# Kernel optimization log

Measured on AMD Instinct MI355X. Metric: run time of the kernel, lower is better.

The kernel has to match this reference:

```python
import jax, jax.numpy as jnp
import numpy as np

B, C, H, W = 32, 1024, 28, 28
TEXT_DIM = 768
ATTN_DIM = 256
REDUCTION = 16
RED = max(1, C // REDUCTION)


def setup_inputs() -> dict:
    key = jax.random.key(0)
    ks = jax.random.split(key, 8)
    x = jax.random.normal(ks[0], (B, C, H, W), dtype=jnp.float32)
    text_feat = jax.random.normal(ks[1], (B, TEXT_DIM), dtype=jnp.float32)
    # ChannelAttention shared MLP (Linear weights, torch layout [out, in], no bias)
    w1 = jax.random.normal(ks[2], (RED, C), dtype=jnp.float32) * (1.0 / np.sqrt(C))
    w2 = jax.random.normal(ks[3], (C, RED), dtype=jnp.float32) * (1.0 / np.sqrt(RED))
    # TextGuidedSpatialAttention projections
    wq = jax.random.normal(ks[4], (ATTN_DIM, TEXT_DIM), dtype=jnp.float32) * 0.001
    wk = jax.random.normal(ks[5], (ATTN_DIM, C), dtype=jnp.float32) * np.sqrt(2.0 / ATTN_DIM)
    wv = jax.random.normal(ks[6], (ATTN_DIM, C), dtype=jnp.float32) * np.sqrt(2.0 / ATTN_DIM)
    wo = jax.random.normal(ks[7], (1, ATTN_DIM), dtype=jnp.float32) * np.sqrt(2.0)
    return {"x": x, "text_feat": text_feat, "w1": w1, "w2": w2,
            "wq": wq, "wk": wk, "wv": wv, "wo": wo}


def _forward(x, text_feat, w1, w2, wq, wk, wv, wo):
    b, c, h, w = x.shape
    # ----- Channel attention -----
    avg = jnp.mean(x, axis=(2, 3))          # [B, C]
    mx = jnp.max(x, axis=(2, 3))            # [B, C]
    def mlp(z):
        return jax.nn.relu(z @ w1.T) @ w2.T  # [B, C]
    ch_attn = jax.nn.sigmoid(mlp(avg) + mlp(mx))   # [B, C]
    x = x * ch_attn[:, :, None, None]
    # ----- Text-guided spatial attention -----
    q = text_feat @ wq.T                     # [B, A]
    # 1x1 conv == channel contraction
    k = jnp.einsum('ac,bchw->bahw', wk, x).reshape(b, ATTN_DIM, h * w)  # [B, A, N]
    v = jnp.einsum('ac,bchw->bahw', wv, x).reshape(b, ATTN_DIM, h * w)  # [B, A, N]
    scores = jnp.einsum('ba,ban->bn', q, k) / jnp.sqrt(jnp.float32(ATTN_DIM))  # [B, N]
    attn_weights = jax.nn.softmax(scores, axis=-1)                      # [B, N]
    attended = jnp.einsum('bn,ban->ba', attn_weights, v)                # [B, A]
    # out_proj 1x1 conv on a spatially-constant tensor == scalar per batch, broadcast
    spatial_scalar = jax.nn.sigmoid(attended @ wo.T)                    # [B, 1]
    spatial_attn = jnp.broadcast_to(spatial_scalar[:, :, None, None], (b, 1, h, w))
    return x * spatial_attn, spatial_attn


def reference(x, text_feat, w1, w2, wq, wk, wv, wo):
    return _forward(x, text_feat, w1, w2, wq, wk, wv, wo)
```

## Files before the change

### kernel.cpp

```cpp
#include <hip/hip_runtime.h>
#include <math.h>

#define B_   32
#define C_   1024
#define N_   784
#define NF4  196
#define TD   768
#define AD   256
#define RED_ 64
#define OUT0 25690112
#define ROWS (B_*C_)
#define CH_  16
#define CPB  64

typedef float f4 __attribute__((ext_vector_type(4)));

#define OFF_AVG 0
#define OFF_MAX 32768
#define OFF_CA  65536
#define OFF_Q   98304
#define OFF_HS  106496
#define OFF_WVO 108544
#define OFF_GQ  109568
#define OFF_SV  142336
#define OFF_CNT 142368
#define OFF_S   142400
#define OFF_Y   167488

__global__ void k_avgmax(const float* __restrict__ x, const float* __restrict__ text,
                         const float* __restrict__ wq, float* __restrict__ avg,
                         float* __restrict__ mx, float* __restrict__ q,
                         int* __restrict__ cnt, float* __restrict__ S,
                         float* __restrict__ Y) {
    int blk = blockIdx.x;
    int wave = threadIdx.x >> 6, lane = threadIdx.x & 63;
    if (blk < 4096) {
        int row0 = blk * 8 + wave * 2;
        const float4* r0 = (const float4*)(x + (size_t)row0 * N_);
        const float4* r1 = r0 + NF4;
        float s0 = 0.f, s1 = 0.f, m0 = -3.4e38f, m1 = -3.4e38f;
        #pragma unroll
        for (int j = 0; j < 3; ++j) {
            int i = lane + 64 * j;
            float4 v0 = r0[i], v1 = r1[i];
            s0 += v0.x + v0.y + v0.z + v0.w;
            s1 += v1.x + v1.y + v1.z + v1.w;
            m0 = fmaxf(m0, fmaxf(fmaxf(v0.x, v0.y), fmaxf(v0.z, v0.w)));
            m1 = fmaxf(m1, fmaxf(fmaxf(v1.x, v1.y), fmaxf(v1.z, v1.w)));
        }
        if (lane < 4) {
            float4 v0 = r0[192 + lane], v1 = r1[192 + lane];
            s0 += v0.x + v0.y + v0.z + v0.w;
            s1 += v1.x + v1.y + v1.z + v1.w;
            m0 = fmaxf(m0, fmaxf(fmaxf(v0.x, v0.y), fmaxf(v0.z, v0.w)));
            m1 = fmaxf(m1, fmaxf(fmaxf(v1.x, v1.y), fmaxf(v1.z, v1.w)));
        }
        for (int o = 32; o; o >>= 1) {
            s0 += __shfl_down(s0, o, 64);
            s1 += __shfl_down(s1, o, 64);
            m0 = fmaxf(m0, __shfl_down(m0, o, 64));
            m1 = fmaxf(m1, __shfl_down(m1, o, 64));
        }
        if (lane == 0) {
            avg[row0]     = s0 * (1.f / (float)N_); mx[row0]     = m0;
            avg[row0 + 1] = s1 * (1.f / (float)N_); mx[row0 + 1] = m1;
        }
    } else if (blk < 6144) {
        int w = (blk - 4096) * 4 + wave;
        int b = w >> 8, a = w & 255;
        const float4* tb = (const float4*)(text + (size_t)b * TD);
        const float4* wr = (const float4*)(wq + (size_t)a * TD);
        float acc = 0.f;
        #pragma unroll
        for (int j = 0; j < 3; ++j) {
            int i = lane + 64 * j;
            float4 tv = tb[i], wvv = wr[i];
            acc += tv.x * wvv.x + tv.y * wvv.y + tv.z * wvv.z + tv.w * wvv.w;
        }
        for (int o = 32; o; o >>= 1) acc += __shfl_down(acc, o, 64);
        if (lane == 0) q[(size_t)b * AD + a] = acc;
    } else if (blk < 6169) {
        int idx = (blk - 6144) * 256 + threadIdx.x;
        if (idx < 6272) {
            f4 z = {0.f, 0.f, 0.f, 0.f};
            ((f4*)S)[idx] = z; ((f4*)Y)[idx] = z;
        }
    } else {
        if (threadIdx.x < B_) cnt[threadIdx.x] = 0;
    }
}

__global__ void k_proj(const float* __restrict__ avg, const float* __restrict__ mx,
                       const float* __restrict__ w1, const float* __restrict__ q,
                       const float* __restrict__ wk, const float* __restrict__ wv,
                       const float* __restrict__ wo, float* __restrict__ hs,
                       float* __restrict__ gq, float* __restrict__ wvo) {
    int blk  = blockIdx.x;
    int wave = threadIdx.x >> 6, lane = threadIdx.x & 63;
    int t = threadIdx.x;
    __shared__ float red[256];
    __shared__ float qs[AD];
    if (blk < 512) {
        int w = blk * 4 + wave;
        int b = w >> 6, r = w & 63;
        const float4* av = (const float4*)(avg + (size_t)b * C_);
        const float4* mv = (const float4*)(mx + (size_t)b * C_);
        const float4* wr = (const float4*)(w1 + (size_t)r * C_);
        float aa = 0.f, am = 0.f;
        #pragma unroll
        for (int j = 0; j < 4; ++j) {
            int i = lane + 64 * j;
            float4 wvv = wr[i], a4 = av[i], m4 = mv[i];
            aa += wvv.x * a4.x + wvv.y * a4.y + wvv.z * a4.z + wvv.w * a4.w;
            am += wvv.x * m4.x + wvv.y * m4.y + wvv.z * m4.z + wvv.w * m4.w;
        }
        for (int o = 32; o; o >>= 1) {
            aa += __shfl_down(aa, o, 64);
            am += __shfl_down(am, o, 64);
        }
        if (lane == 0) hs[(size_t)b * RED_ + r] = fmaxf(aa, 0.f) + fmaxf(am, 0.f);
    } else if (blk < 1024) {
        int local = blk - 512;
        int b  = local >> 4, cb = local & 15;
        int cl = t & 63, sl = t >> 6;
        int c  = cb * 64 + cl;
        qs[t] = q[(size_t)b * AD + t];
        __syncthreads();
        const float* wkp = wk + (size_t)(sl * 64) * C_ + c;
        float acc = 0.f;
        #pragma unroll 8
        for (int a = 0; a < 64; ++a) acc += qs[sl * 64 + a] * wkp[(size_t)a * C_];
        red[t] = acc;
        __syncthreads();
        if (t < 64) gq[(size_t)b * C_ + c] = red[t] + red[64 + t] + red[128 + t] + red[192 + t];
    } else {
        int local = blk - 1024;
        int cl = t & 63, sl = t >> 6;
        int c = local * 64 + cl;
        const float* wvp = wv + (size_t)(sl * 64) * C_ + c;
        float acc = 0.f;
        #pragma unroll 8
        for (int a = 0; a < 64; ++a) acc += wo[sl * 64 + a] * wvp[(size_t)a * C_];
        red[t] = acc;
        __syncthreads();
        if (t < 64) wvo[local * 64 + t] = red[t] + red[64 + t] + red[128 + t] + red[192 + t];
    }
}

__global__ __launch_bounds__(256, 4) void k_scores(
        const float* __restrict__ x, const float* __restrict__ hs,
        const float* __restrict__ w2, const float* __restrict__ gq,
        const float* __restrict__ wvo,
        float* __restrict__ ca, float* __restrict__ S, float* __restrict__ Y,
        int* __restrict__ cnt, float* __restrict__ sv) {
    int chunk = blockIdx.x;
    int bh    = blockIdx.y;
    int b = bh >> 1, half = bh & 1;
    int t = threadIdx.x;
    int wave = t >> 6, lane = t & 63;
    __shared__ float hss[RED_];
    __shared__ float redB[256];
    __shared__ float gsg[CPB], gsh[CPB];
    __shared__ f4 l4s[392], l4y[392];
    __shared__ float rm[4], rs[4], rd[4];
    __shared__ int winflag;

    if (t < RED_) hss[t] = hs[(size_t)b * RED_ + t];
    __syncthreads();
    {
        int cl = t & 63, sl = t >> 6;
        int c  = chunk * CPB + cl;
        const float* w2p = w2 + (size_t)c * RED_ + sl * 16;
        float a1 = 0.f;
        #pragma unroll
        for (int r = 0; r < 16; ++r) a1 += hss[sl * 16 + r] * w2p[r];
        redB[t] = a1;
    }
    __syncthreads();
    if (t < CPB) {
        float s1 = redB[t] + redB[64 + t] + redB[128 + t] + redB[192 + t];
        float cav = 1.f / (1.f + __expf(-s1));
        int c = chunk * CPB + t;
        ca[(size_t)b * C_ + c] = cav;
        gsg[t] = gq[(size_t)b * C_ + c] * cav * 0.0625f;
        gsh[t] = wvo[c] * cav;
    }
    __syncthreads();
    const f4* xb4 = (const f4*)(x +
        ((size_t)b * C_ + (size_t)chunk * CPB + (size_t)wave * 16) * N_) + (size_t)half * 98;
    f4 sA = {0,0,0,0}, sB = {0,0,0,0}, yA = {0,0,0,0}, yB = {0,0,0,0};
    #pragma unroll 4
    for (int cc = 0; cc < 16; ++cc) {
        float gv = gsg[wave * 16 + cc], hv = gsh[wave * 16 + cc];
        const f4* row = xb4 + (size_t)cc * NF4;
        f4 v = row[lane];
        sA += gv * v; yA += hv * v;
        if (lane < 34) {
            f4 v2 = row[64 + lane];
            sB += gv * v2; yB += hv * v2;
        }
    }
    l4s[wave * 98 + lane] = sA; l4y[wave * 98 + lane] = yA;
    if (lane < 34) { l4s[wave * 98 + 64 + lane] = sB; l4y[wave * 98 + 64 + lane] = yB; }
    __syncthreads();
    if (t < 98) {
        f4 rsv = l4s[t] + l4s[98 + t] + l4s[196 + t] + l4s[294 + t];
        f4 ryv = l4y[t] + l4y[98 + t] + l4y[196 + t] + l4y[294 + t];
        float* Sp = S + (size_t)b * N_ + half * 392 + t * 4;
        float* Yp = Y + (size_t)b * N_ + half * 392 + t * 4;
        atomicAdd(Sp + 0, rsv.x); atomicAdd(Sp + 1, rsv.y);
        atomicAdd(Sp + 2, rsv.z); atomicAdd(Sp + 3, rsv.w);
        atomicAdd(Yp + 0, ryv.x); atomicAdd(Yp + 1, ryv.y);
        atomicAdd(Yp + 2, ryv.z); atomicAdd(Yp + 3, ryv.w);
    }
    __syncthreads();
    if (t == 0) {
        __threadfence();
        winflag = (atomicAdd(&cnt[b], 1) == 2 * CH_ - 1) ? 1 : 0;
    }
    __syncthreads();
    if (!winflag) return;
    __threadfence();
    const float* Sb = S + (size_t)b * N_;
    const float* Yb = Y + (size_t)b * N_;
    float v0 = Sb[t], v1 = Sb[t + 256], v2 = Sb[t + 512];
    float v3 = (t < 16) ? Sb[t + 768] : -3.4e38f;
    float m = fmaxf(fmaxf(v0, v1), fmaxf(v2, v3));
    for (int o = 32; o; o >>= 1) m = fmaxf(m, __shfl_down(m, o, 64));
    if (lane == 0) rm[wave] = m;
    __syncthreads();
    float M = fmaxf(fmaxf(rm[0], rm[1]), fmaxf(rm[2], rm[3]));
    float e0 = __expf(v0 - M), e1 = __expf(v1 - M), e2 = __expf(v2 - M);
    float e3 = (t < 16) ? __expf(v3 - M) : 0.f;
    float w0 = Yb[t], w1v = Yb[t + 256], w2v = Yb[t + 512];
    float w3 = (t < 16) ? Yb[t + 768] : 0.f;
    float ssum = e0 + e1 + e2 + e3;
    float dot  = e0 * w0 + e1 * w1v + e2 * w2v + e3 * w3;
    for (int o = 32; o; o >>= 1) {
        ssum += __shfl_down(ssum, o, 64);
        dot  += __shfl_down(dot,  o, 64);
    }
    if (lane == 0) { rs[wave] = ssum; rd[wave] = dot; }
    __syncthreads();
    if (t == 0) {
        float Ssum = rs[0] + rs[1] + rs[2] + rs[3];
        float Dsum = rd[0] + rd[1] + rd[2] + rd[3];
        sv[b] = 1.f / (1.f + __expf(-Dsum / Ssum));
    }
}

__global__ void k_finalize(const float* __restrict__ x, const float* __restrict__ chattn,
                           const float* __restrict__ s, float* __restrict__ out) {
    int blk = blockIdx.x;
    if (blk < ROWS / 8) {
        int wave = threadIdx.x >> 6, lane = threadIdx.x & 63;
        int row0 = blk * 8 + wave * 2;
        int b    = row0 >> 10;
        float sb  = s[b];
        float sc0 = chattn[row0] * sb;
        float sc1 = chattn[row0 + 1] * sb;
        const float4* r0 = (const float4*)(x + (size_t)row0 * N_);
        const float4* r1 = r0 + NF4;
        f4* o0 = (f4*)(out + (size_t)row0 * N_);
        f4* o1 = o0 + NF4;
        #pragma unroll
        for (int j = 0; j < 3; ++j) {
            int i = lane + 64 * j;
            float4 v0 = r0[i], v1 = r1[i];
            f4 w0 = { v0.x * sc0, v0.y * sc0, v0.z * sc0, v0.w * sc0 };
            f4 w1 = { v1.x * sc1, v1.y * sc1, v1.z * sc1, v1.w * sc1 };
            __builtin_nontemporal_store(w0, &o0[i]);
            __builtin_nontemporal_store(w1, &o1[i]);
        }
        if (lane < 4) {
            int i = 192 + lane;
            float4 v0 = r0[i], v1 = r1[i];
            f4 w0 = { v0.x * sc0, v0.y * sc0, v0.z * sc0, v0.w * sc0 };
            f4 w1 = { v1.x * sc1, v1.y * sc1, v1.z * sc1, v1.w * sc1 };
            __builtin_nontemporal_store(w0, &o0[i]);
            __builtin_nontemporal_store(w1, &o1[i]);
        }
    } else {
        int idx = (blk - ROWS / 8) * 256 + threadIdx.x;
        if (idx < (B_ * N_) / 4) {
            int b = idx / (N_ / 4);
            float v = s[b];
            f4 vv = { v, v, v, v };
            __builtin_nontemporal_store(vv, &((f4*)(out + OUT0))[idx]);
        }
    }
}

extern "C" void kernel_launch(void* const* d_in, const int* in_sizes, int n_in,
                              void* d_out, int out_size, void* d_ws, size_t ws_size,
                              hipStream_t stream) {
    const float* x    = (const float*)d_in[0];
    const float* text = (const float*)d_in[1];
    const float* w1   = (const float*)d_in[2];
    const float* w2   = (const float*)d_in[3];
    const float* wq   = (const float*)d_in[4];
    const float* wk   = (const float*)d_in[5];
    const float* wv   = (const float*)d_in[6];
    const float* wo   = (const float*)d_in[7];
    float* out = (float*)d_out;
    float* ws  = (float*)d_ws;

    float* avg = ws + OFF_AVG;
    float* mx  = ws + OFF_MAX;
    float* ca  = ws + OFF_CA;
    float* q   = ws + OFF_Q;
    float* hs  = ws + OFF_HS;
    float* wvo = ws + OFF_WVO;
    float* gq  = ws + OFF_GQ;
    float* sv  = ws + OFF_SV;
    int*   cnt = (int*)(ws + OFF_CNT);
    float* S   = ws + OFF_S;
    float* Y   = ws + OFF_Y;

    k_avgmax<<<6170, 256, 0, stream>>>(x, text, wq, avg, mx, q, cnt, S, Y);
    k_proj<<<1040, 256, 0, stream>>>(avg, mx, w1, q, wk, wv, wo, hs, gq, wvo);
    k_scores<<<dim3(CH_, B_ * 2), 256, 0, stream>>>(x, hs, w2, gq, wvo, ca, S, Y, cnt, sv);
    k_finalize<<<ROWS / 8 + 25, 256, 0, stream>>>(x, ca, sv, out);
}
```

Baseline: 264.3 us.

## Fuse finalize into scores kernel with per-batch spin-wait on softmax result

Drops the separate finalize kernel. Each scores block now covers full rows of 64 channels of one batch instead of half rows, and after the softmax winner publishes the spatial scalar through a flag, every block of that batch spins on the flag, then re-reads its x slice (likely still in cache) and writes the scaled output directly. This removes one kernel launch and a full extra pass that read x and the channel-attention buffer from memory. The cost is an inter-block spin-wait that deadlocks unless all 16 blocks of a batch are co-resident. There are 512 blocks, and the occupancy hint was removed while 16 f4 loads are held in registers per lane.

After: 283.7 us. 1.07x slower.

```diff
diff --git a/kernel.cpp b/kernel.cpp
--- a/kernel.cpp
+++ b/kernel.cpp
@@ -15,23 +15,23 @@
 
 typedef float f4 __attribute__((ext_vector_type(4)));
 
-#define OFF_AVG 0
-#define OFF_MAX 32768
-#define OFF_CA  65536
-#define OFF_Q   98304
-#define OFF_HS  106496
-#define OFF_WVO 108544
-#define OFF_GQ  109568
-#define OFF_SV  142336
-#define OFF_CNT 142368
-#define OFF_S   142400
-#define OFF_Y   167488
+#define OFF_AVG  0
+#define OFF_MAX  32768
+#define OFF_Q    65536
+#define OFF_HS   73728
+#define OFF_WVO  75776
+#define OFF_GQ   76800
+#define OFF_SV   109568
+#define OFF_CNT  109600
+#define OFF_FLAG 109632
+#define OFF_S    109664
+#define OFF_Y    134752
 
 __global__ void k_avgmax(const float* __restrict__ x, const float* __restrict__ text,
                          const float* __restrict__ wq, float* __restrict__ avg,
                          float* __restrict__ mx, float* __restrict__ q,
-                         int* __restrict__ cnt, float* __restrict__ S,
-                         float* __restrict__ Y) {
+                         int* __restrict__ cnt, int* __restrict__ flag,
+                         float* __restrict__ S, float* __restrict__ Y) {
     int blk = blockIdx.x;
     int wave = threadIdx.x >> 6, lane = threadIdx.x & 63;
     if (blk < 4096) {
@@ -86,7 +86,8 @@
             ((f4*)S)[idx] = z; ((f4*)Y)[idx] = z;
         }
     } else {
-        if (threadIdx.x < B_) cnt[threadIdx.x] = 0;
+        if (threadIdx.x < B_)            cnt[threadIdx.x] = 0;
+        else if (threadIdx.x < 2 * B_)   flag[threadIdx.x - B_] = 0;
     }
 }
 
@@ -147,22 +148,20 @@
     }
 }
 
-__global__ __launch_bounds__(256, 4) void k_scores(
+__global__ __launch_bounds__(256) void k_scores(
         const float* __restrict__ x, const float* __restrict__ hs,
         const float* __restrict__ w2, const float* __restrict__ gq,
-        const float* __restrict__ wvo,
-        float* __restrict__ ca, float* __restrict__ S, float* __restrict__ Y,
-        int* __restrict__ cnt, float* __restrict__ sv) {
-    int chunk = blockIdx.x;
-    int bh    = blockIdx.y;
-    int b = bh >> 1, half = bh & 1;
-    int t = threadIdx.x;
+        const float* __restrict__ wvo, float* __restrict__ S,
+        float* __restrict__ Y, int* __restrict__ cnt, int* __restrict__ flag,
+        float* __restrict__ sv, float* __restrict__ out) {
+    int chunk = blockIdx.x, b = blockIdx.y, t = threadIdx.x;
     int wave = t >> 6, lane = t & 63;
     __shared__ float hss[RED_];
     __shared__ float redB[256];
-    __shared__ float gsg[CPB], gsh[CPB];
-    __shared__ f4 l4s[392], l4y[392];
+    __shared__ float gsg[CPB], gsh[CPB], cavs[CPB];
+    __shared__ f4 l4s[4 * NF4], l4y[4 * NF4];
     __shared__ float rm[4], rs[4], rd[4];
+    __shared__ float svs;
     __shared__ int winflag;
 
     if (t < RED_) hss[t] = hs[(size_t)b * RED_ + t];
@@ -180,34 +179,48 @@
     if (t < CPB) {
         float s1 = redB[t] + redB[64 + t] + redB[128 + t] + redB[192 + t];
         float cav = 1.f / (1.f + __expf(-s1));
-        int c = chunk * CPB + t;
-        ca[(size_t)b * C_ + c] = cav;
-        gsg[t] = gq[(size_t)b * C_ + c] * cav * 0.0625f;
-        gsh[t] = wvo[c] * cav;
+        cavs[t] = cav;
+        gsg[t] = gq[(size_t)b * C_ + chunk * CPB + t] * cav * 0.0625f;
+        gsh[t] = wvo[chunk * CPB + t] * cav;
     }
     __syncthreads();
     const f4* xb4 = (const f4*)(x +
-        ((size_t)b * C_ + (size_t)chunk * CPB + (size_t)wave * 16) * N_) + (size_t)half * 98;
-    f4 sA = {0,0,0,0}, sB = {0,0,0,0}, yA = {0,0,0,0}, yB = {0,0,0,0};
-    #pragma unroll 4
-    for (int cc = 0; cc < 16; ++cc) {
-        float gv = gsg[wave * 16 + cc], hv = gsh[wave * 16 + cc];
-        const f4* row = xb4 + (size_t)cc * NF4;
-        f4 v = row[lane];
-        sA += gv * v; yA += hv * v;
-        if (lane < 34) {
-            f4 v2 = row[64 + lane];
-            sB += gv * v2; yB += hv * v2;
-        }
-    }
-    l4s[wave * 98 + lane] = sA; l4y[wave * 98 + lane] = yA;
-    if (lane < 34) { l4s[wave * 98 + 64 + lane] = sB; l4y[wave * 98 + 64 + lane] = yB; }
-    __syncthreads();
-    if (t < 98) {
-        f4 rsv = l4s[t] + l4s[98 + t] + l4s[196 + t] + l4s[294 + t];
-        f4 ryv = l4y[t] + l4y[98 + t] + l4y[196 + t] + l4y[294 + t];
-        float* Sp = S + (size_t)b * N_ + half * 392 + t * 4;
-        float* Yp = Y + (size_t)b * N_ + half * 392 + t * 4;
+        ((size_t)b * C_ + (size_t)chunk * CPB + (size_t)wave * 16) * N_);
+    #pragma unroll
+    for (int slot = 0; slot < 3; ++slot) {
+        int i = lane + 64 * slot;
+        f4 v[16];
+        #pragma unroll
+        for (int cc = 0; cc < 16; ++cc) v[cc] = xb4[(size_t)cc * NF4 + i];
+        f4 vs = {0,0,0,0}, vy = {0,0,0,0};
+        #pragma unroll
+        for (int cc = 0; cc < 16; ++cc) {
+            vs += gsg[wave * 16 + cc] * v[cc];
+            vy += gsh[wave * 16 + cc] * v[cc];
+        }
+        l4s[wave * NF4 + i] = vs;
+        l4y[wave * NF4 + i] = vy;
+    }
+    if (lane < 4) {
+        int i = 192 + lane;
+        f4 v[16];
+        #pragma unroll
+        for (int cc = 0; cc < 16; ++cc) v[cc] = xb4[(size_t)cc * NF4 + i];
+        f4 vs = {0,0,0,0}, vy = {0,0,0,0};
+        #pragma unroll
+        for (int cc = 0; cc < 16; ++cc) {
+            vs += gsg[wave * 16 + cc] * v[cc];
+            vy += gsh[wave * 16 + cc] * v[cc];
+        }
+        l4s[wave * NF4 + i] = vs;
+        l4y[wave * NF4 + i] = vy;
+    }
+    __syncthreads();
+    if (t < NF4) {
+        f4 rsv = l4s[t] + l4s[NF4 + t] + l4s[2 * NF4 + t] + l4s[3 * NF4 + t];
+        f4 ryv = l4y[t] + l4y[NF4 + t] + l4y[2 * NF4 + t] + l4y[3 * NF4 + t];
+        float* Sp = S + (size_t)b * N_ + t * 4;
+        float* Yp = Y + (size_t)b * N_ + t * 4;
         atomicAdd(Sp + 0, rsv.x); atomicAdd(Sp + 1, rsv.y);
         atomicAdd(Sp + 2, rsv.z); atomicAdd(Sp + 3, rsv.w);
         atomicAdd(Yp + 0, ryv.x); atomicAdd(Yp + 1, ryv.y);
@@ -216,77 +229,78 @@
     __syncthreads();
     if (t == 0) {
         __threadfence();
-        winflag = (atomicAdd(&cnt[b], 1) == 2 * CH_ - 1) ? 1 : 0;
-    }
-    __syncthreads();
-    if (!winflag) return;
-    __threadfence();
-    const float* Sb = S + (size_t)b * N_;
-    const float* Yb = Y + (size_t)b * N_;
-    float v0 = Sb[t], v1 = Sb[t + 256], v2 = Sb[t + 512];
-    float v3 = (t < 16) ? Sb[t + 768] : -3.4e38f;
-    float m = fmaxf(fmaxf(v0, v1), fmaxf(v2, v3));
-    for (int o = 32; o; o >>= 1) m = fmaxf(m, __shfl_down(m, o, 64));
-    if (lane == 0) rm[wave] = m;
-    __syncthreads();
-    float M = fmaxf(fmaxf(rm[0], rm[1]), fmaxf(rm[2], rm[3]));
-    float e0 = __expf(v0 - M), e1 = __expf(v1 - M), e2 = __expf(v2 - M);
-    float e3 = (t < 16) ? __expf(v3 - M) : 0.f;
-    float w0 = Yb[t], w1v = Yb[t + 256], w2v = Yb[t + 512];
-    float w3 = (t < 16) ? Yb[t + 768] : 0.f;
-    float ssum = e0 + e1 + e2 + e3;
-    float dot  = e0 * w0 + e1 * w1v + e2 * w2v + e3 * w3;
-    for (int o = 32; o; o >>= 1) {
-        ssum += __shfl_down(ssum, o, 64);
-        dot  += __shfl_down(dot,  o, 64);
-    }
-    if (lane == 0) { rs[wave] = ssum; rd[wave] = dot; }
-    __syncthreads();
-    if (t == 0) {
-        float Ssum = rs[0] + rs[1] + rs[2] + rs[3];
-        float Dsum = rd[0] + rd[1] + rd[2] + rd[3];
-        sv[b] = 1.f / (1.f + __expf(-Dsum / Ssum));
-    }
-}
-
-__global__ void k_finalize(const float* __restrict__ x, const float* __restrict__ chattn,
-                           const float* __restrict__ s, float* __restrict__ out) {
-    int blk = blockIdx.x;
-    if (blk < ROWS / 8) {
-        int wave = threadIdx.x >> 6, lane = threadIdx.x & 63;
-        int row0 = blk * 8 + wave * 2;
-        int b    = row0 >> 10;
-        float sb  = s[b];
-        float sc0 = chattn[row0] * sb;
-        float sc1 = chattn[row0 + 1] * sb;
-        const float4* r0 = (const float4*)(x + (size_t)row0 * N_);
-        const float4* r1 = r0 + NF4;
-        f4* o0 = (f4*)(out + (size_t)row0 * N_);
-        f4* o1 = o0 + NF4;
-        #pragma unroll
-        for (int j = 0; j < 3; ++j) {
-            int i = lane + 64 * j;
-            float4 v0 = r0[i], v1 = r1[i];
-            f4 w0 = { v0.x * sc0, v0.y * sc0, v0.z * sc0, v0.w * sc0 };
-            f4 w1 = { v1.x * sc1, v1.y * sc1, v1.z * sc1, v1.w * sc1 };
-            __builtin_nontemporal_store(w0, &o0[i]);
-            __builtin_nontemporal_store(w1, &o1[i]);
-        }
-        if (lane < 4) {
-            int i = 192 + lane;
-            float4 v0 = r0[i], v1 = r1[i];
-            f4 w0 = { v0.x * sc0, v0.y * sc0, v0.z * sc0, v0.w * sc0 };
-            f4 w1 = { v1.x * sc1, v1.y * sc1, v1.z * sc1, v1.w * sc1 };
-            __builtin_nontemporal_store(w0, &o0[i]);
-            __builtin_nontemporal_store(w1, &o1[i]);
+        winflag = (atomicAdd(&cnt[b], 1) == CH_ - 1) ? 1 : 0;
+    }
+    __syncthreads();
+    if (winflag) {
+        __threadfence();
+        const float* Sb = S + (size_t)b * N_;
+        const float* Yb = Y + (size_t)b * N_;
+        float v0 = Sb[t], v1 = Sb[t + 256], v2 = Sb[t + 512];
+        float v3 = (t < 16) ? Sb[t + 768] : -3.4e38f;
+        float m = fmaxf(fmaxf(v0, v1), fmaxf(v2, v3));
+        for (int o = 32; o; o >>= 1) m = fmaxf(m, __shfl_down(m, o, 64));
+        if (lane == 0) rm[wave] = m;
+        __syncthreads();
+        float M = fmaxf(fmaxf(rm[0], rm[1]), fmaxf(rm[2], rm[3]));
+        float e0 = __expf(v0 - M), e1 = __expf(v1 - M), e2 = __expf(v2 - M);
+        float e3 = (t < 16) ? __expf(v3 - M) : 0.f;
+        float w0 = Yb[t], w1v = Yb[t + 256], w2v = Yb[t + 512];
+        float w3 = (t < 16) ? Yb[t + 768] : 0.f;
+        float ssum = e0 + e1 + e2 + e3;
+        float dot  = e0 * w0 + e1 * w1v + e2 * w2v + e3 * w3;
+        for (int o = 32; o; o >>= 1) {
+            ssum += __shfl_down(ssum, o, 64);
+            dot  += __shfl_down(dot,  o, 64);
+        }
+        if (lane == 0) { rs[wave] = ssum; rd[wave] = dot; }
+        __syncthreads();
+        if (t == 0) {
+            float Ssum = rs[0] + rs[1] + rs[2] + rs[3];
+            float Dsum = rd[0] + rd[1] + rd[2] + rd[3];
+            float sb = 1.f / (1.f + __expf(-Dsum / Ssum));
+            sv[b] = sb; svs = sb;
+            __threadfence();
+            atomicExch(&flag[b], 1);
+        }
+        __syncthreads();
+        if (t < NF4) {
+            float svb = svs;
+            f4 vv = {svb, svb, svb, svb};
+            __builtin_nontemporal_store(vv, &((f4*)(out + OUT0))[b * NF4 + t]);
         }
     } else {
-        int idx = (blk - ROWS / 8) * 256 + threadIdx.x;
-        if (idx < (B_ * N_) / 4) {
-            int b = idx / (N_ / 4);
-            float v = s[b];
-            f4 vv = { v, v, v, v };
-            __builtin_nontemporal_store(vv, &((f4*)(out + OUT0))[idx]);
+        if (t == 0) {
+            while (atomicCAS(&flag[b], 1, 1) != 1) { }
+            __threadfence();
+            svs = sv[b];
+        }
+        __syncthreads();
+    }
+    float svb = svs;
+    f4* ob4 = (f4*)(out +
+        ((size_t)b * C_ + (size_t)chunk * CPB + (size_t)wave * 16) * N_);
+    #pragma unroll
+    for (int slot = 0; slot < 3; ++slot) {
+        int i = lane + 64 * slot;
+        f4 v[16];
+        #pragma unroll
+        for (int cc = 0; cc < 16; ++cc) v[cc] = xb4[(size_t)cc * NF4 + i];
+        #pragma unroll
+        for (int cc = 0; cc < 16; ++cc) {
+            f4 o = v[cc] * (cavs[wave * 16 + cc] * svb);
+            __builtin_nontemporal_store(o, &ob4[(size_t)cc * NF4 + i]);
+        }
+    }
+    if (lane < 4) {
+        int i = 192 + lane;
+        f4 v[16];
+        #pragma unroll
+        for (int cc = 0; cc < 16; ++cc) v[cc] = xb4[(size_t)cc * NF4 + i];
+        #pragma unroll
+        for (int cc = 0; cc < 16; ++cc) {
+            f4 o = v[cc] * (cavs[wave * 16 + cc] * svb);
+            __builtin_nontemporal_store(o, &ob4[(size_t)cc * NF4 + i]);
         }
     }
 }
@@ -305,20 +319,19 @@
     float* out = (float*)d_out;
     float* ws  = (float*)d_ws;
 
-    float* avg = ws + OFF_AVG;
-    float* mx  = ws + OFF_MAX;
-    float* ca  = ws + OFF_CA;
-    float* q   = ws + OFF_Q;
-    float* hs  = ws + OFF_HS;
-    float* wvo = ws + OFF_WVO;
-    float* gq  = ws + OFF_GQ;
-    float* sv  = ws + OFF_SV;
-    int*   cnt = (int*)(ws + OFF_CNT);
-    float* S   = ws + OFF_S;
-    float* Y   = ws + OFF_Y;
-
-    k_avgmax<<<6170, 256, 0, stream>>>(x, text, wq, avg, mx, q, cnt, S, Y);
+    float* avg  = ws + OFF_AVG;
+    float* mx   = ws + OFF_MAX;
+    float* q    = ws + OFF_Q;
+    float* hs   = ws + OFF_HS;
+    float* wvo  = ws + OFF_WVO;
+    float* gq   = ws + OFF_GQ;
+    float* sv   = ws + OFF_SV;
+    int*   cnt  = (int*)(ws + OFF_CNT);
+    int*   flag = (int*)(ws + OFF_FLAG);
+    float* S    = ws + OFF_S;
+    float* Y    = ws + OFF_Y;
+
+    k_avgmax<<<6170, 256, 0, stream>>>(x, text, wq, avg, mx, q, cnt, flag, S, Y);
     k_proj<<<1040, 256, 0, stream>>>(avg, mx, w1, q, wk, wv, wo, hs, gq, wvo);
-    k_scores<<<dim3(CH_, B_ * 2), 256, 0, stream>>>(x, hs, w2, gq, wvo, ca, S, Y, cnt, sv);
-    k_finalize<<<ROWS / 8 + 25, 256, 0, stream>>>(x, ca, sv, out);
+    k_scores<<<dim3(CH_, B_), 256, 0, stream>>>(x, hs, w2, gq, wvo, S, Y, cnt, flag, sv, out);
 }
```

## Fold projection kernel into avgmax and scores kernels, drop spatial half split

Applied to the files above, without the earlier changes.

Removes the separate k_proj launch. The wv·wo reduction moves into k_avgmax as extra blocks, and the w1 MLP and the wk·q projection are computed inside each k_scores block. k_scores now covers the full spatial row per block instead of two halves, and it batches 16 channel loads per slot to raise memory-level parallelism. The trade-off is redundant work: every chunk block recomputes the full 64-row w1 MLP for its batch. Halving the grid to 512 blocks also lowers occupancy.

Measured after the change: 273.7 us. 3.6% more time.

```diff
diff --git a/kernel.cpp b/kernel.cpp
--- a/kernel.cpp
+++ b/kernel.cpp
@@ -15,25 +15,26 @@
 
 typedef float f4 __attribute__((ext_vector_type(4)));
 
-#define OFF_AVG 0
-#define OFF_MAX 32768
-#define OFF_CA  65536
-#define OFF_Q   98304
-#define OFF_HS  106496
-#define OFF_WVO 108544
-#define OFF_GQ  109568
-#define OFF_SV  142336
-#define OFF_CNT 142368
-#define OFF_S   142400
-#define OFF_Y   167488
+#define OFF_AVG  0
+#define OFF_MAX  32768
+#define OFF_CA   65536
+#define OFF_Q    98304
+#define OFF_WVO  106496
+#define OFF_SV   107520
+#define OFF_CNT  107552
+#define OFF_S    107584
+#define OFF_Y    132672
 
 __global__ void k_avgmax(const float* __restrict__ x, const float* __restrict__ text,
-                         const float* __restrict__ wq, float* __restrict__ avg,
+                         const float* __restrict__ wq, const float* __restrict__ wv,
+                         const float* __restrict__ wo, float* __restrict__ avg,
                          float* __restrict__ mx, float* __restrict__ q,
-                         int* __restrict__ cnt, float* __restrict__ S,
-                         float* __restrict__ Y) {
+                         float* __restrict__ wvo, int* __restrict__ cnt,
+                         float* __restrict__ S, float* __restrict__ Y) {
     int blk = blockIdx.x;
     int wave = threadIdx.x >> 6, lane = threadIdx.x & 63;
+    int t = threadIdx.x;
+    __shared__ float red[256];
     if (blk < 4096) {
         int row0 = blk * 8 + wave * 2;
         const float4* r0 = (const float4*)(x + (size_t)row0 * N_);
@@ -80,61 +81,13 @@
         for (int o = 32; o; o >>= 1) acc += __shfl_down(acc, o, 64);
         if (lane == 0) q[(size_t)b * AD + a] = acc;
     } else if (blk < 6169) {
-        int idx = (blk - 6144) * 256 + threadIdx.x;
+        int idx = (blk - 6144) * 256 + t;
         if (idx < 6272) {
             f4 z = {0.f, 0.f, 0.f, 0.f};
             ((f4*)S)[idx] = z; ((f4*)Y)[idx] = z;
         }
-    } else {
-        if (threadIdx.x < B_) cnt[threadIdx.x] = 0;
-    }
-}
-
-__global__ void k_proj(const float* __restrict__ avg, const float* __restrict__ mx,
-                       const float* __restrict__ w1, const float* __restrict__ q,
-                       const float* __restrict__ wk, const float* __restrict__ wv,
-                       const float* __restrict__ wo, float* __restrict__ hs,
-                       float* __restrict__ gq, float* __restrict__ wvo) {
-    int blk  = blockIdx.x;
-    int wave = threadIdx.x >> 6, lane = threadIdx.x & 63;
-    int t = threadIdx.x;
-    __shared__ float red[256];
-    __shared__ float qs[AD];
-    if (blk < 512) {
-        int w = blk * 4 + wave;
-        int b = w >> 6, r = w & 63;
-        const float4* av = (const float4*)(avg + (size_t)b * C_);
-        const float4* mv = (const float4*)(mx + (size_t)b * C_);
-        const float4* wr = (const float4*)(w1 + (size_t)r * C_);
-        float aa = 0.f, am = 0.f;
-        #pragma unroll
-        for (int j = 0; j < 4; ++j) {
-            int i = lane + 64 * j;
-            float4 wvv = wr[i], a4 = av[i], m4 = mv[i];
-            aa += wvv.x * a4.x + wvv.y * a4.y + wvv.z * a4.z + wvv.w * a4.w;
-            am += wvv.x * m4.x + wvv.y * m4.y + wvv.z * m4.z + wvv.w * m4.w;
-        }
-        for (int o = 32; o; o >>= 1) {
-            aa += __shfl_down(aa, o, 64);
-            am += __shfl_down(am, o, 64);
-        }
-        if (lane == 0) hs[(size_t)b * RED_ + r] = fmaxf(aa, 0.f) + fmaxf(am, 0.f);
-    } else if (blk < 1024) {
-        int local = blk - 512;
-        int b  = local >> 4, cb = local & 15;
-        int cl = t & 63, sl = t >> 6;
-        int c  = cb * 64 + cl;
-        qs[t] = q[(size_t)b * AD + t];
-        __syncthreads();
-        const float* wkp = wk + (size_t)(sl * 64) * C_ + c;
-        float acc = 0.f;
-        #pragma unroll 8
-        for (int a = 0; a < 64; ++a) acc += qs[sl * 64 + a] * wkp[(size_t)a * C_];
-        red[t] = acc;
-        __syncthreads();
-        if (t < 64) gq[(size_t)b * C_ + c] = red[t] + red[64 + t] + red[128 + t] + red[192 + t];
-    } else {
-        int local = blk - 1024;
+    } else if (blk < 6185) {
+        int local = blk - 6169;
         int cl = t & 63, sl = t >> 6;
         int c = local * 64 + cl;
         const float* wvp = wv + (size_t)(sl * 64) * C_ + c;
@@ -144,70 +97,111 @@
         red[t] = acc;
         __syncthreads();
         if (t < 64) wvo[local * 64 + t] = red[t] + red[64 + t] + red[128 + t] + red[192 + t];
+    } else {
+        if (t < B_) cnt[t] = 0;
     }
 }
 
-__global__ __launch_bounds__(256, 4) void k_scores(
-        const float* __restrict__ x, const float* __restrict__ hs,
-        const float* __restrict__ w2, const float* __restrict__ gq,
-        const float* __restrict__ wvo,
+__global__ __launch_bounds__(256) void k_scores(
+        const float* __restrict__ x, const float* __restrict__ avg,
+        const float* __restrict__ mx, const float* __restrict__ w1,
+        const float* __restrict__ w2, const float* __restrict__ q,
+        const float* __restrict__ wk, const float* __restrict__ wvo,
         float* __restrict__ ca, float* __restrict__ S, float* __restrict__ Y,
         int* __restrict__ cnt, float* __restrict__ sv) {
-    int chunk = blockIdx.x;
-    int bh    = blockIdx.y;
-    int b = bh >> 1, half = bh & 1;
-    int t = threadIdx.x;
+    int chunk = blockIdx.x, b = blockIdx.y, t = threadIdx.x;
     int wave = t >> 6, lane = t & 63;
+    __shared__ float qs[AD];
+    __shared__ float redA[256];
     __shared__ float hss[RED_];
-    __shared__ float redB[256];
     __shared__ float gsg[CPB], gsh[CPB];
-    __shared__ f4 l4s[392], l4y[392];
+    __shared__ f4 l4s[4 * NF4], l4y[4 * NF4];
     __shared__ float rm[4], rs[4], rd[4];
     __shared__ int winflag;
 
-    if (t < RED_) hss[t] = hs[(size_t)b * RED_ + t];
+    qs[t] = q[(size_t)b * AD + t];
     __syncthreads();
     {
         int cl = t & 63, sl = t >> 6;
-        int c  = chunk * CPB + cl;
-        const float* w2p = w2 + (size_t)c * RED_ + sl * 16;
-        float a1 = 0.f;
-        #pragma unroll
-        for (int r = 0; r < 16; ++r) a1 += hss[sl * 16 + r] * w2p[r];
-        redB[t] = a1;
+        int c = chunk * CPB + cl;
+        const float* wkp = wk + (size_t)(sl * 64) * C_ + c;
+        float acc = 0.f;
+        #pragma unroll 8
+        for (int a = 0; a < 64; ++a) acc += qs[sl * 64 + a] * wkp[(size_t)a * C_];
+        redA[t] = acc;
+    }
+    {
+        const f4* av = (const f4*)(avg + (size_t)b * C_);
+        const f4* mv = (const f4*)(mx + (size_t)b * C_);
+        for (int rr = 0; rr < 16; ++rr) {
+            int r = wave * 16 + rr;
+            const f4* wr = (const f4*)(w1 + (size_t)r * C_);
+            float aa = 0.f, am = 0.f;
+            #pragma unroll
+            for (int j = 0; j < 4; ++j) {
+                int i = lane + 64 * j;
+                f4 wv4 = wr[i], a4 = av[i], m4 = mv[i];
+                aa += wv4.x * a4.x + wv4.y * a4.y + wv4.z * a4.z + wv4.w * a4.w;
+                am += wv4.x * m4.x + wv4.y * m4.y + wv4.z * m4.z + wv4.w * m4.w;
+            }
+            for (int o = 32; o; o >>= 1) {
+                aa += __shfl_down(aa, o, 64);
+                am += __shfl_down(am, o, 64);
+            }
+            if (lane == 0) hss[r] = fmaxf(aa, 0.f) + fmaxf(am, 0.f);
+        }
     }
     __syncthreads();
     if (t < CPB) {
-        float s1 = redB[t] + redB[64 + t] + redB[128 + t] + redB[192 + t];
+        int c = chunk * CPB + t;
+        const float* w2p = w2 + (size_t)c * RED_;
+        float s1 = 0.f;
+        #pragma unroll 8
+        for (int r = 0; r < RED_; ++r) s1 += hss[r] * w2p[r];
         float cav = 1.f / (1.f + __expf(-s1));
-        int c = chunk * CPB + t;
         ca[(size_t)b * C_ + c] = cav;
-        gsg[t] = gq[(size_t)b * C_ + c] * cav * 0.0625f;
+        float gqv = redA[t] + redA[64 + t] + redA[128 + t] + redA[192 + t];
+        gsg[t] = gqv * cav * 0.0625f;
         gsh[t] = wvo[c] * cav;
     }
     __syncthreads();
     const f4* xb4 = (const f4*)(x +
-        ((size_t)b * C_ + (size_t)chunk * CPB + (size_t)wave * 16) * N_) + (size_t)half * 98;
-    f4 sA = {0,0,0,0}, sB = {0,0,0,0}, yA = {0,0,0,0}, yB = {0,0,0,0};
-    #pragma unroll 4
-    for (int cc = 0; cc < 16; ++cc) {
-        float gv = gsg[wave * 16 + cc], hv = gsh[wave * 16 + cc];
-        const f4* row = xb4 + (size_t)cc * NF4;
-        f4 v = row[lane];
-        sA += gv * v; yA += hv * v;
-        if (lane < 34) {
-            f4 v2 = row[64 + lane];
-            sB += gv * v2; yB += hv * v2;
-        }
-    }
-    l4s[wave * 98 + lane] = sA; l4y[wave * 98 + lane] = yA;
-    if (lane < 34) { l4s[wave * 98 + 64 + lane] = sB; l4y[wave * 98 + 64 + lane] = yB; }
-    __syncthreads();
-    if (t < 98) {
-        f4 rsv = l4s[t] + l4s[98 + t] + l4s[196 + t] + l4s[294 + t];
-        f4 ryv = l4y[t] + l4y[98 + t] + l4y[196 + t] + l4y[294 + t];
-        float* Sp = S + (size_t)b * N_ + half * 392 + t * 4;
-        float* Yp = Y + (size_t)b * N_ + half * 392 + t * 4;
+        ((size_t)b * C_ + (size_t)chunk * CPB + (size_t)wave * 16) * N_);
+    #pragma unroll
+    for (int slot = 0; slot < 3; ++slot) {
+        int i = lane + 64 * slot;
+        f4 v[16];
+        #pragma unroll
+        for (int cc = 0; cc < 16; ++cc) v[cc] = xb4[(size_t)cc * NF4 + i];
+        f4 vs = {0,0,0,0}, vy = {0,0,0,0};
+        #pragma unroll
+        for (int cc = 0; cc < 16; ++cc) {
+            vs += gsg[wave * 16 + cc] * v[cc];
+            vy += gsh[wave * 16 + cc] * v[cc];
+        }
+        l4s[wave * NF4 + i] = vs;
+        l4y[wave * NF4 + i] = vy;
+    }
+    if (lane < 4) {
+        int i = 192 + lane;
+        f4 v[16];
+        #pragma unroll
+        for (int cc = 0; cc < 16; ++cc) v[cc] = xb4[(size_t)cc * NF4 + i];
+        f4 vs = {0,0,0,0}, vy = {0,0,0,0};
+        #pragma unroll
+        for (int cc = 0; cc < 16; ++cc) {
+            vs += gsg[wave * 16 + cc] * v[cc];
+            vy += gsh[wave * 16 + cc] * v[cc];
+        }
+        l4s[wave * NF4 + i] = vs;
+        l4y[wave * NF4 + i] = vy;
+    }
+    __syncthreads();
+    if (t < NF4) {
+        f4 rsv = l4s[t] + l4s[NF4 + t] + l4s[2 * NF4 + t] + l4s[3 * NF4 + t];
+        f4 ryv = l4y[t] + l4y[NF4 + t] + l4y[2 * NF4 + t] + l4y[3 * NF4 + t];
+        float* Sp = S + (size_t)b * N_ + t * 4;
+        float* Yp = Y + (size_t)b * N_ + t * 4;
         atomicAdd(Sp + 0, rsv.x); atomicAdd(Sp + 1, rsv.y);
         atomicAdd(Sp + 2, rsv.z); atomicAdd(Sp + 3, rsv.w);
         atomicAdd(Yp + 0, ryv.x); atomicAdd(Yp + 1, ryv.y);
@@ -216,7 +210,7 @@
     __syncthreads();
     if (t == 0) {
         __threadfence();
-        winflag = (atomicAdd(&cnt[b], 1) == 2 * CH_ - 1) ? 1 : 0;
+        winflag = (atomicAdd(&cnt[b], 1) == CH_ - 1) ? 1 : 0;
     }
     __syncthreads();
     if (!winflag) return;
@@ -309,16 +303,13 @@
     float* mx  = ws + OFF_MAX;
     float* ca  = ws + OFF_CA;
     float* q   = ws + OFF_Q;
-    float* hs  = ws + OFF_HS;
     float* wvo = ws + OFF_WVO;
-    float* gq  = ws + OFF_GQ;
     float* sv  = ws + OFF_SV;
     int*   cnt = (int*)(ws + OFF_CNT);
     float* S   = ws + OFF_S;
     float* Y   = ws + OFF_Y;
 
-    k_avgmax<<<6170, 256, 0, stream>>>(x, text, wq, avg, mx, q, cnt, S, Y);
-    k_proj<<<1040, 256, 0, stream>>>(avg, mx, w1, q, wk, wv, wo, hs, gq, wvo);
-    k_scores<<<dim3(CH_, B_ * 2), 256, 0, stream>>>(x, hs, w2, gq, wvo, ca, S, Y, cnt, sv);
+    k_avgmax<<<6186, 256, 0, stream>>>(x, text, wq, wv, wo, avg, mx, q, wvo, cnt, S, Y);
+    k_scores<<<dim3(CH_, B_), 256, 0, stream>>>(x, avg, mx, w1, w2, q, wk, wvo, ca, S, Y, cnt, sv);
     k_finalize<<<ROWS / 8 + 25, 256, 0, stream>>>(x, ca, sv, out);
 }
```

## Split score pass into three spatial slices per chunk and move wvo into first kernel

Applied to the files above, without the earlier changes.

The k_scores kernel now splits each batch's spatial dimension into three slices of 64 float4 columns (the last slice also takes a 4-column tail) instead of two halves. This gives every lane a single load per channel instead of a partial second load, and raises the grid to 48x32 blocks. The wv·wo projection is moved from k_proj into k_avgmax, since it does not depend on the reductions. The costs are that the channel-MLP prologue is recomputed three times per chunk instead of twice, and more atomic adds and counter increments are issued per batch. The launch-bounds occupancy hint is also dropped.

Measured after the change: 293.1 us. 1.11x slower.

```diff
diff --git a/kernel.cpp b/kernel.cpp
--- a/kernel.cpp
+++ b/kernel.cpp
@@ -12,28 +12,32 @@
 #define ROWS (B_*C_)
 #define CH_  16
 #define CPB  64
+#define NSL  3
 
 typedef float f4 __attribute__((ext_vector_type(4)));
 
-#define OFF_AVG 0
-#define OFF_MAX 32768
-#define OFF_CA  65536
-#define OFF_Q   98304
-#define OFF_HS  106496
-#define OFF_WVO 108544
-#define OFF_GQ  109568
-#define OFF_SV  142336
-#define OFF_CNT 142368
-#define OFF_S   142400
-#define OFF_Y   167488
+#define OFF_AVG  0
+#define OFF_MAX  32768
+#define OFF_CA   65536
+#define OFF_Q    98304
+#define OFF_HS   106496
+#define OFF_WVO  108544
+#define OFF_GQ   109568
+#define OFF_SV   142336
+#define OFF_CNT  142368
+#define OFF_S    142400
+#define OFF_Y    167488
 
 __global__ void k_avgmax(const float* __restrict__ x, const float* __restrict__ text,
-                         const float* __restrict__ wq, float* __restrict__ avg,
+                         const float* __restrict__ wq, const float* __restrict__ wv,
+                         const float* __restrict__ wo, float* __restrict__ avg,
                          float* __restrict__ mx, float* __restrict__ q,
-                         int* __restrict__ cnt, float* __restrict__ S,
-                         float* __restrict__ Y) {
+                         float* __restrict__ wvo, int* __restrict__ cnt,
+                         float* __restrict__ S, float* __restrict__ Y) {
     int blk = blockIdx.x;
     int wave = threadIdx.x >> 6, lane = threadIdx.x & 63;
+    int t = threadIdx.x;
+    __shared__ float red[256];
     if (blk < 4096) {
         int row0 = blk * 8 + wave * 2;
         const float4* r0 = (const float4*)(x + (size_t)row0 * N_);
@@ -80,21 +84,31 @@
         for (int o = 32; o; o >>= 1) acc += __shfl_down(acc, o, 64);
         if (lane == 0) q[(size_t)b * AD + a] = acc;
     } else if (blk < 6169) {
-        int idx = (blk - 6144) * 256 + threadIdx.x;
+        int idx = (blk - 6144) * 256 + t;
         if (idx < 6272) {
             f4 z = {0.f, 0.f, 0.f, 0.f};
             ((f4*)S)[idx] = z; ((f4*)Y)[idx] = z;
         }
+    } else if (blk < 6185) {
+        int local = blk - 6169;
+        int cl = t & 63, sl = t >> 6;
+        int c = local * 64 + cl;
+        const float* wvp = wv + (size_t)(sl * 64) * C_ + c;
+        float acc = 0.f;
+        #pragma unroll 8
+        for (int a = 0; a < 64; ++a) acc += wo[sl * 64 + a] * wvp[(size_t)a * C_];
+        red[t] = acc;
+        __syncthreads();
+        if (t < 64) wvo[local * 64 + t] = red[t] + red[64 + t] + red[128 + t] + red[192 + t];
     } else {
-        if (threadIdx.x < B_) cnt[threadIdx.x] = 0;
+        if (t < B_) cnt[t] = 0;
     }
 }
 
 __global__ void k_proj(const float* __restrict__ avg, const float* __restrict__ mx,
                        const float* __restrict__ w1, const float* __restrict__ q,
-                       const float* __restrict__ wk, const float* __restrict__ wv,
-                       const float* __restrict__ wo, float* __restrict__ hs,
-                       float* __restrict__ gq, float* __restrict__ wvo) {
+                       const float* __restrict__ wk, float* __restrict__ hs,
+                       float* __restrict__ gq) {
     int blk  = blockIdx.x;
     int wave = threadIdx.x >> 6, lane = threadIdx.x & 63;
     int t = threadIdx.x;
@@ -119,7 +133,7 @@
             am += __shfl_down(am, o, 64);
         }
         if (lane == 0) hs[(size_t)b * RED_ + r] = fmaxf(aa, 0.f) + fmaxf(am, 0.f);
-    } else if (blk < 1024) {
+    } else {
         int local = blk - 512;
         int b  = local >> 4, cb = local & 15;
         int cl = t & 63, sl = t >> 6;
@@ -133,35 +147,23 @@
         red[t] = acc;
         __syncthreads();
         if (t < 64) gq[(size_t)b * C_ + c] = red[t] + red[64 + t] + red[128 + t] + red[192 + t];
-    } else {
-        int local = blk - 1024;
-        int cl = t & 63, sl = t >> 6;
-        int c = local * 64 + cl;
-        const float* wvp = wv + (size_t)(sl * 64) * C_ + c;
-        float acc = 0.f;
-        #pragma unroll 8
-        for (int a = 0; a < 64; ++a) acc += wo[sl * 64 + a] * wvp[(size_t)a * C_];
-        red[t] = acc;
-        __syncthreads();
-        if (t < 64) wvo[local * 64 + t] = red[t] + red[64 + t] + red[128 + t] + red[192 + t];
-    }
-}
-
-__global__ __launch_bounds__(256, 4) void k_scores(
+    }
+}
+
+__global__ __launch_bounds__(256) void k_scores(
         const float* __restrict__ x, const float* __restrict__ hs,
         const float* __restrict__ w2, const float* __restrict__ gq,
         const float* __restrict__ wvo,
         float* __restrict__ ca, float* __restrict__ S, float* __restrict__ Y,
         int* __restrict__ cnt, float* __restrict__ sv) {
-    int chunk = blockIdx.x;
-    int bh    = blockIdx.y;
-    int b = bh >> 1, half = bh & 1;
-    int t = threadIdx.x;
+    int bx = blockIdx.x;
+    int chunk = bx / NSL, s = bx - chunk * NSL;
+    int b = blockIdx.y, t = threadIdx.x;
     int wave = t >> 6, lane = t & 63;
     __shared__ float hss[RED_];
     __shared__ float redB[256];
     __shared__ float gsg[CPB], gsh[CPB];
-    __shared__ f4 l4s[392], l4y[392];
+    __shared__ f4 l4s[4 * 68], l4y[4 * 68];
     __shared__ float rm[4], rs[4], rd[4];
     __shared__ int winflag;
 
@@ -181,33 +183,36 @@
         float s1 = redB[t] + redB[64 + t] + redB[128 + t] + redB[192 + t];
         float cav = 1.f / (1.f + __expf(-s1));
         int c = chunk * CPB + t;
-        ca[(size_t)b * C_ + c] = cav;
+        if (s == 0) ca[(size_t)b * C_ + c] = cav;
         gsg[t] = gq[(size_t)b * C_ + c] * cav * 0.0625f;
         gsh[t] = wvo[c] * cav;
     }
     __syncthreads();
     const f4* xb4 = (const f4*)(x +
-        ((size_t)b * C_ + (size_t)chunk * CPB + (size_t)wave * 16) * N_) + (size_t)half * 98;
-    f4 sA = {0,0,0,0}, sB = {0,0,0,0}, yA = {0,0,0,0}, yB = {0,0,0,0};
+        ((size_t)b * C_ + (size_t)chunk * CPB + (size_t)wave * 16) * N_);
+    int base = s * 64;
+    bool tail = (s == 2) && (lane < 4);
+    f4 vs = {0,0,0,0}, vy = {0,0,0,0}, vs2 = {0,0,0,0}, vy2 = {0,0,0,0};
     #pragma unroll 4
     for (int cc = 0; cc < 16; ++cc) {
         float gv = gsg[wave * 16 + cc], hv = gsh[wave * 16 + cc];
         const f4* row = xb4 + (size_t)cc * NF4;
-        f4 v = row[lane];
-        sA += gv * v; yA += hv * v;
-        if (lane < 34) {
-            f4 v2 = row[64 + lane];
-            sB += gv * v2; yB += hv * v2;
-        }
-    }
-    l4s[wave * 98 + lane] = sA; l4y[wave * 98 + lane] = yA;
-    if (lane < 34) { l4s[wave * 98 + 64 + lane] = sB; l4y[wave * 98 + 64 + lane] = yB; }
-    __syncthreads();
-    if (t < 98) {
-        f4 rsv = l4s[t] + l4s[98 + t] + l4s[196 + t] + l4s[294 + t];
-        f4 ryv = l4y[t] + l4y[98 + t] + l4y[196 + t] + l4y[294 + t];
-        float* Sp = S + (size_t)b * N_ + half * 392 + t * 4;
-        float* Yp = Y + (size_t)b * N_ + half * 392 + t * 4;
+        f4 v = row[base + lane];
+        vs += gv * v; vy += hv * v;
+        if (tail) {
+            f4 v2 = row[192 + lane];
+            vs2 += gv * v2; vy2 += hv * v2;
+        }
+    }
+    l4s[wave * 68 + lane] = vs;  l4y[wave * 68 + lane] = vy;
+    if (tail) { l4s[wave * 68 + 64 + lane] = vs2; l4y[wave * 68 + 64 + lane] = vy2; }
+    __syncthreads();
+    int NW = (s == 2) ? 68 : 64;
+    if (t < NW) {
+        f4 rsv = l4s[t] + l4s[68 + t] + l4s[136 + t] + l4s[204 + t];
+        f4 ryv = l4y[t] + l4y[68 + t] + l4y[136 + t] + l4y[204 + t];
+        float* Sp = S + (size_t)b * N_ + (base + t) * 4;
+        float* Yp = Y + (size_t)b * N_ + (base + t) * 4;
         atomicAdd(Sp + 0, rsv.x); atomicAdd(Sp + 1, rsv.y);
         atomicAdd(Sp + 2, rsv.z); atomicAdd(Sp + 3, rsv.w);
         atomicAdd(Yp + 0, ryv.x); atomicAdd(Yp + 1, ryv.y);
@@ -216,7 +221,7 @@
     __syncthreads();
     if (t == 0) {
         __threadfence();
-        winflag = (atomicAdd(&cnt[b], 1) == 2 * CH_ - 1) ? 1 : 0;
+        winflag = (atomicAdd(&cnt[b], 1) == CH_ * NSL - 1) ? 1 : 0;
     }
     __syncthreads();
     if (!winflag) return;
@@ -317,8 +322,8 @@
     float* S   = ws + OFF_S;
     float* Y   = ws + OFF_Y;
 
-    k_avgmax<<<6170, 256, 0, stream>>>(x, text, wq, avg, mx, q, cnt, S, Y);
-    k_proj<<<1040, 256, 0, stream>>>(avg, mx, w1, q, wk, wv, wo, hs, gq, wvo);
-    k_scores<<<dim3(CH_, B_ * 2), 256, 0, stream>>>(x, hs, w2, gq, wvo, ca, S, Y, cnt, sv);
+    k_avgmax<<<6186, 256, 0, stream>>>(x, text, wq, wv, wo, avg, mx, q, wvo, cnt, S, Y);
+    k_proj<<<1024, 256, 0, stream>>>(avg, mx, w1, q, wk, hs, gq);
+    k_scores<<<dim3(CH_ * NSL, B_), 256, 0, stream>>>(x, hs, w2, gq, wvo, ca, S, Y, cnt, sv);
     k_finalize<<<ROWS / 8 + 25, 256, 0, stream>>>(x, ca, sv, out);
 }
```
